# Optimization experiments

Hardware: AMD Instinct MI355X
Metric: run time of the kernel (lower is better)

The kernel has to match this reference:

```python
import jax, jax.numpy as jnp
import numpy as np

B, S, H = 2, 1024, 2048
E, I, K = 32, 768, 4


def setup_inputs() -> dict:
    key = jax.random.key(0)
    k1, k2, k3, k4, k5 = jax.random.split(key, 5)
    sH = 1.0 / np.sqrt(H)
    sI = 1.0 / np.sqrt(I)
    return {
        "hidden_states": jax.random.normal(k1, (B, S, H), dtype=jnp.float32),
        "gate_w": jax.random.normal(k2, (E, H), dtype=jnp.float32) * sH,
        "w_gate": jax.random.normal(k3, (E, H, I), dtype=jnp.float32) * sH,
        "w_up": jax.random.normal(k4, (E, H, I), dtype=jnp.float32) * sH,
        "w_down": jax.random.normal(k5, (E, I, H), dtype=jnp.float32) * sI,
        "top_k": K,
    }


def reference(hidden_states, gate_w, w_gate, w_up, w_down, top_k):
    b, s, h = hidden_states.shape
    x = hidden_states.reshape(-1, h)                      # [T, H]
    T = x.shape[0]

    # Router: logits -> softmax over experts -> top-k -> renormalize
    logits = x @ gate_w.T                                 # [T, E]
    probs = jax.nn.softmax(logits, axis=-1)
    topv, topi = jax.lax.top_k(probs, top_k)              # [T, K]
    topv = topv / jnp.sum(topv, axis=-1, keepdims=True)   # norm_topk_prob

    # Dense routing-weight matrix (zero except selected experts) [T, E]
    rw = jnp.zeros((T, probs.shape[-1]), dtype=x.dtype)
    rw = rw.at[jnp.arange(T)[:, None], topi].set(topv)

    # Expert SwiGLU MLPs, computed for all experts then masked-combined
    g = jnp.einsum('th,ehi->eti', x, w_gate)              # [E, T, I]
    u = jnp.einsum('th,ehi->eti', x, w_up)                # [E, T, I]
    act = jax.nn.silu(g) * u                              # [E, T, I]
    expert_out = jnp.einsum('eti,eih->eth', act, w_down)  # [E, T, H]

    out = jnp.einsum('te,eth->th', rw, expert_out)        # combine [T, H]
    return out.reshape(b, s, h).astype(hidden_states.dtype)
```

## Files before the change

### kernel.cpp

```cpp
#include <hip/hip_runtime.h>
#include <hip/hip_bf16.h>
#include <math.h>

typedef unsigned short u16;
typedef unsigned int u32;
typedef unsigned long long u64;
typedef short s16x8 __attribute__((ext_vector_type(8)));
typedef u32 u32x2 __attribute__((ext_vector_type(2)));
typedef u32 u32x4 __attribute__((ext_vector_type(4)));
typedef float f32x4 __attribute__((ext_vector_type(4)));

#define TTOK 2048
#define HDIM 2048
#define ENUM 32
#define IDIM 768
#define KTOP 4

#define WS_XB   0L
#define WS_ACT  8388608L
#define WS_TIDX 20971520L
#define WS_TW   (WS_TIDX + 32768L)
#define WS_CNT  (WS_TW + 32768L)
#define WS_OFFS (WS_CNT + 128L)
#define WS_CUR  (WS_OFFS + 256L)
#define WS_RTOK (WS_CUR + 128L)
#define WS_RW   (WS_RTOK + 32768L)

#define LDBW 20

__device__ __forceinline__ u16 f2bf(float f) {
  unsigned u = __builtin_bit_cast(unsigned, f);
  unsigned r = (u + 0x7fffu + ((u >> 16) & 1u)) >> 16;
  return (u16)r;
}

__device__ __forceinline__ u32 cvtpk(float lo, float hi) {
  u32 r;
  asm("v_cvt_pk_bf16_f32 %0, %1, %2" : "=v"(r) : "v"(lo), "v"(hi));
  return r;
}

__device__ __forceinline__ void gll16(const void* g, void* l) {
  u32 loff = __builtin_amdgcn_readfirstlane((u32)(u64)l);
  __builtin_amdgcn_global_load_lds(
      (const __attribute__((address_space(1))) u32*)(u64)g,
      (__attribute__((address_space(3))) u32*)loff, 16, 0, 0);
}

__device__ __forceinline__ s16x8 bfrag(const u32* B, int d0, int d1) {
  u32x2 lo = *(const u32x2*)(B + d0);
  u32x2 hi = *(const u32x2*)(B + d1);
  u32x4 v = {lo.x, lo.y, hi.x, hi.y};
  return __builtin_bit_cast(s16x8, v);
}

__global__ __launch_bounds__(256) void router_kernel(const float* __restrict__ x,
                                                     const float* __restrict__ gw,
                                                     u16* __restrict__ xb,
                                                     int* __restrict__ tidx,
                                                     float* __restrict__ tw,
                                                     int* __restrict__ counts) {
  __shared__ float xs[HDIM];
  __shared__ float part[256];
  __shared__ float lg[ENUM];
  int t = blockIdx.x;
  const float4* xr = (const float4*)(x + (long)t * HDIM);
  float4* xs4 = (float4*)xs;
  for (int i = threadIdx.x; i < HDIM / 4; i += 256) xs4[i] = xr[i];
  __syncthreads();
  {
    int i0 = threadIdx.x * 8;
    uint4 o;
    o.x = cvtpk(xs[i0], xs[i0 + 1]);
    o.y = cvtpk(xs[i0 + 2], xs[i0 + 3]);
    o.z = cvtpk(xs[i0 + 4], xs[i0 + 5]);
    o.w = cvtpk(xs[i0 + 6], xs[i0 + 7]);
    *(uint4*)(xb + (long)t * HDIM + i0) = o;
  }
  int e = threadIdx.x >> 3, ch = threadIdx.x & 7;
  const float4* gp = (const float4*)(gw + (long)e * HDIM + ch * 256);
  const float4* xp = (const float4*)(xs + ch * 256);
  float s = 0.f;
#pragma unroll 8
  for (int c = 0; c < 64; c++) {
    float4 gv = gp[c], xv = xp[c];
    s += gv.x * xv.x + gv.y * xv.y + gv.z * xv.z + gv.w * xv.w;
  }
  part[threadIdx.x] = s;
  __syncthreads();
  if (threadIdx.x < 32) {
    float v = 0.f;
#pragma unroll
    for (int j = 0; j < 8; j++) v += part[threadIdx.x * 8 + j];
    lg[threadIdx.x] = v;
  }
  __syncthreads();
  if (threadIdx.x == 0) {
    int sel[KTOP]; float sv[KTOP];
    unsigned mask = 0;
    for (int k = 0; k < KTOP; k++) {
      float best = -INFINITY; int bi = 0;
      for (int j = 0; j < ENUM; j++)
        if (!((mask >> j) & 1u) && lg[j] > best) { best = lg[j]; bi = j; }
      mask |= 1u << bi; sel[k] = bi; sv[k] = best;
    }
    float m = sv[0], den = 0.f, ex[KTOP];
    for (int k = 0; k < KTOP; k++) { ex[k] = expf(sv[k] - m); den += ex[k]; }
    for (int k = 0; k < KTOP; k++) {
      tidx[t * KTOP + k] = sel[k];
      tw[t * KTOP + k] = ex[k] / den;
      atomicAdd(&counts[sel[k]], 1);
    }
  }
}

__global__ void scan_kernel(const int* __restrict__ counts, int* __restrict__ offs,
                            int* __restrict__ cur) {
  if (threadIdx.x == 0) {
    int a = 0;
    for (int e = 0; e < ENUM; e++) { offs[e] = a; a += counts[e]; }
    offs[ENUM] = a;
  }
  if (threadIdx.x < ENUM) cur[threadIdx.x] = 0;
}

__global__ __launch_bounds__(256) void scatter_kernel(const int* __restrict__ tidx,
                                                      const float* __restrict__ tw,
                                                      const int* __restrict__ offs,
                                                      int* __restrict__ cur,
                                                      int* __restrict__ rtok,
                                                      float* __restrict__ rw) {
  int i = blockIdx.x * 256 + threadIdx.x;
  int e = tidx[i];
  int pos = atomicAdd(&cur[e], 1);
  int row = offs[e] + pos;
  rtok[row] = i >> 2;
  rw[row] = tw[i];
}

__global__ __launch_bounds__(512) void gemm1_kernel(const u16* __restrict__ xb,
                                                    const float* __restrict__ wgp,
                                                    const float* __restrict__ wup,
                                                    const int* __restrict__ offs,
                                                    const int* __restrict__ rtok,
                                                    u16* __restrict__ act) {
  int d = blockIdx.x;
  int e = d & 31;
  int nt = (d >> 5) % 12;
  int mt = d / 384;
  int off = offs[e], cnt = offs[e + 1] - off;
  int m0 = mt << 8;
  if (m0 >= cnt) return;
  int rows = cnt - m0; if (rows > 256) rows = 256;
  int baser = off + m0;
  int n0 = nt << 6;

  __shared__ __align__(16) u16 As[2][256 * 32];
  __shared__ __align__(16) u32 Bs[2][2][64 * LDBW];

  int tid = threadIdx.x;
  int ln = tid & 63, w = tid >> 6;
  int wm = w >> 1, wn = w & 1;
  int lhi = ln >> 4, llo = ln & 15;

  const u16* gA[2];
  int ldsA[2];
#pragma unroll
  for (int j = 0; j < 2; j++) {
    int idx = w * 2 + j;
    int r = idx * 16 + (ln >> 2);
    int c = ln & 3;
    int csrc = c ^ ((r >> 1) & 3);
    int rr = r < rows ? r : rows - 1;
    gA[j] = xb + (long)rtok[baser + rr] * HDIM + csrc * 8;
    ldsA[j] = idx * 1024;
  }

  int mat = tid >> 8;
  int t2 = tid & 255;
  int a = t2 & 15;
  int kk = t2 >> 4;
  const float* gB = (mat ? wup : wgp) + (long)e * ((long)HDIM * IDIM) +
                    (long)(2 * kk) * IDIM + n0 + 4 * a;
  int fB = 2 * (a & 7);
  int wOff[4];
#pragma unroll
  for (int j = 0; j < 4; j++) wOff[j] = (4 * a + j) * LDBW + (kk ^ fB);

  int offA[4];
#pragma unroll
  for (int mf = 0; mf < 4; mf++) {
    int r = wm * 64 + mf * 16 + llo;
    offA[mf] = r * 64 + ((lhi ^ ((r >> 1) & 3)) * 16);
  }
  int dB0[2], dB1[2];
#pragma unroll
  for (int nf = 0; nf < 2; nf++) {
    int n = wn * 32 + nf * 16 + llo;
    int f = 2 * ((n >> 2) & 7);
    dB0[nf] = n * LDBW + ((4 * lhi) ^ f);
    dB1[nf] = n * LDBW + (((4 * lhi) | 2) ^ f);
  }

  f32x4 accg[4][2], accu[4][2];
  f32x4 zz = {0.f, 0.f, 0.f, 0.f};
#pragma unroll
  for (int i = 0; i < 4; i++)
#pragma unroll
    for (int j = 0; j < 2; j++) { accg[i][j] = zz; accu[i][j] = zz; }

  float4 rB0, rB1;

  rB0 = *(const float4*)gB;
  rB1 = *(const float4*)(gB + IDIM);
  gll16(gA[0], (char*)As[0] + ldsA[0]);
  gll16(gA[1], (char*)As[0] + ldsA[1]);
  {
    u32* bb = &Bs[0][mat][0];
    bb[wOff[0]] = cvtpk(rB0.x, rB1.x);
    bb[wOff[1]] = cvtpk(rB0.y, rB1.y);
    bb[wOff[2]] = cvtpk(rB0.z, rB1.z);
    bb[wOff[3]] = cvtpk(rB0.w, rB1.w);
  }
  __syncthreads();

  const int NS = HDIM / 32;
  int buf = 0;
  for (int t = 0; t < NS; ++t) {
    if (t + 1 < NS) {
      const float* p = gB + (long)(t + 1) * 32 * IDIM;
      rB0 = *(const float4*)p;
      rB1 = *(const float4*)(p + IDIM);
      gll16(gA[0] + (t + 1) * 32, (char*)As[buf ^ 1] + ldsA[0]);
      gll16(gA[1] + (t + 1) * 32, (char*)As[buf ^ 1] + ldsA[1]);
    }
    __builtin_amdgcn_sched_barrier(0);
    {
      const char* Ab = (const char*)As[buf];
      const u32* Bg = &Bs[buf][0][0];
      const u32* Bu = &Bs[buf][1][0];
      s16x8 av[4];
#pragma unroll
      for (int mf = 0; mf < 4; mf++) av[mf] = *(const s16x8*)(Ab + offA[mf]);
#pragma unroll
      for (int nf = 0; nf < 2; nf++) {
        s16x8 bg = bfrag(Bg, dB0[nf], dB1[nf]);
        s16x8 bu = bfrag(Bu, dB0[nf], dB1[nf]);
#pragma unroll
        for (int mf = 0; mf < 4; mf++) {
          accg[mf][nf] = __builtin_amdgcn_mfma_f32_16x16x32_bf16(av[mf], bg, accg[mf][nf], 0, 0, 0);
          accu[mf][nf] = __builtin_amdgcn_mfma_f32_16x16x32_bf16(av[mf], bu, accu[mf][nf], 0, 0, 0);
        }
      }
    }
    if (t + 1 < NS) {
      u32* bb = &Bs[buf ^ 1][mat][0];
      bb[wOff[0]] = cvtpk(rB0.x, rB1.x);
      bb[wOff[1]] = cvtpk(rB0.y, rB1.y);
      bb[wOff[2]] = cvtpk(rB0.z, rB1.z);
      bb[wOff[3]] = cvtpk(rB0.w, rB1.w);
    }
    __syncthreads();
    buf ^= 1;
  }

  int rb = wm * 64 + lhi * 4;
  int cb = n0 + wn * 32 + llo;
#pragma unroll
  for (int mf = 0; mf < 4; mf++) {
#pragma unroll
    for (int r4 = 0; r4 < 4; r4++) {
      int rl = rb + mf * 16 + r4;
      if (rl < rows) {
        long rowb = (long)(baser + rl) * IDIM;
#pragma unroll
        for (int nf = 0; nf < 2; nf++) {
          float g = accg[mf][nf][r4], u = accu[mf][nf][r4];
          float av = g / (1.f + __expf(-g)) * u;
          act[rowb + cb + nf * 16] = f2bf(av);
        }
      }
    }
  }
}

__global__ __launch_bounds__(512) void gemm2_kernel(const u16* __restrict__ act,
                                                    const float* __restrict__ wdp,
                                                    const int* __restrict__ offs,
                                                    const int* __restrict__ rtok,
                                                    const float* __restrict__ rw,
                                                    float* __restrict__ out) {
  int d = blockIdx.x;
  int e = d & 31;
  int nt = (d >> 5) & 31;
  int mt = d >> 10;
  int off = offs[e], cnt = offs[e + 1] - off;
  int m0 = mt << 8;
  if (m0 >= cnt) return;
  int rows = cnt - m0; if (rows > 256) rows = 256;
  int baser = off + m0;
  int n0 = nt << 6;

  __shared__ __align__(16) u16 As[2][256 * 32];
  __shared__ __align__(16) u32 Bs[2][64 * LDBW];

  int tid = threadIdx.x;
  int ln = tid & 63, w = tid >> 6;
  int wm = w >> 1, wn = w & 1;
  int lhi = ln >> 4, llo = ln & 15;

  const u16* gA[2];
  int ldsA[2];
#pragma unroll
  for (int j = 0; j < 2; j++) {
    int idx = w * 2 + j;
    int r = idx * 16 + (ln >> 2);
    int c = ln & 3;
    int csrc = c ^ ((r >> 1) & 3);
    int rr = r < rows ? r : rows - 1;
    gA[j] = act + (long)(baser + rr) * IDIM + csrc * 8;
    ldsA[j] = idx * 1024;
  }

  int isB = (tid < 256);
  int a = tid & 15;
  int kk = (tid >> 4) & 15;
  const float* gB = wdp + (long)e * ((long)IDIM * HDIM) +
                    (long)(2 * kk) * HDIM + n0 + 4 * a;
  int fB = 2 * (a & 7);
  int wOff[4];
#pragma unroll
  for (int j = 0; j < 4; j++) wOff[j] = (4 * a + j) * LDBW + (kk ^ fB);

  int offA[4];
#pragma unroll
  for (int mf = 0; mf < 4; mf++) {
    int r = wm * 64 + mf * 16 + llo;
    offA[mf] = r * 64 + ((lhi ^ ((r >> 1) & 3)) * 16);
  }
  int dB0[2], dB1[2];
#pragma unroll
  for (int nf = 0; nf < 2; nf++) {
    int n = wn * 32 + nf * 16 + llo;
    int f = 2 * ((n >> 2) & 7);
    dB0[nf] = n * LDBW + ((4 * lhi) ^ f);
    dB1[nf] = n * LDBW + (((4 * lhi) | 2) ^ f);
  }

  f32x4 acc[4][2];
  f32x4 zz = {0.f, 0.f, 0.f, 0.f};
#pragma unroll
  for (int i = 0; i < 4; i++)
#pragma unroll
    for (int j = 0; j < 2; j++) acc[i][j] = zz;

  float4 rB0, rB1;

  if (isB) {
    rB0 = *(const float4*)gB;
    rB1 = *(const float4*)(gB + HDIM);
  }
  gll16(gA[0], (char*)As[0] + ldsA[0]);
  gll16(gA[1], (char*)As[0] + ldsA[1]);
  if (isB) {
    u32* bb = &Bs[0][0];
    bb[wOff[0]] = cvtpk(rB0.x, rB1.x);
    bb[wOff[1]] = cvtpk(rB0.y, rB1.y);
    bb[wOff[2]] = cvtpk(rB0.z, rB1.z);
    bb[wOff[3]] = cvtpk(rB0.w, rB1.w);
  }
  __syncthreads();

  const int NS = IDIM / 32;
  int buf = 0;
  for (int t = 0; t < NS; ++t) {
    if (t + 1 < NS) {
      if (isB) {
        const float* p = gB + (long)(t + 1) * 32 * HDIM;
        rB0 = *(const float4*)p;
        rB1 = *(const float4*)(p + HDIM);
      }
      gll16(gA[0] + (t + 1) * 32, (char*)As[buf ^ 1] + ldsA[0]);
      gll16(gA[1] + (t + 1) * 32, (char*)As[buf ^ 1] + ldsA[1]);
    }
    __builtin_amdgcn_sched_barrier(0);
    {
      const char* Ab = (const char*)As[buf];
      const u32* Bb = &Bs[buf][0];
      s16x8 av[4];
#pragma unroll
      for (int mf = 0; mf < 4; mf++) av[mf] = *(const s16x8*)(Ab + offA[mf]);
#pragma unroll
      for (int nf = 0; nf < 2; nf++) {
        s16x8 bv = bfrag(Bb, dB0[nf], dB1[nf]);
#pragma unroll
        for (int mf = 0; mf < 4; mf++)
          acc[mf][nf] = __builtin_amdgcn_mfma_f32_16x16x32_bf16(av[mf], bv, acc[mf][nf], 0, 0, 0);
      }
    }
    if (t + 1 < NS && isB) {
      u32* bb = &Bs[buf ^ 1][0];
      bb[wOff[0]] = cvtpk(rB0.x, rB1.x);
      bb[wOff[1]] = cvtpk(rB0.y, rB1.y);
      bb[wOff[2]] = cvtpk(rB0.z, rB1.z);
      bb[wOff[3]] = cvtpk(rB0.w, rB1.w);
    }
    __syncthreads();
    buf ^= 1;
  }

  int rb = wm * 64 + lhi * 4;
  int cb = n0 + wn * 32 + llo;
#pragma unroll
  for (int mf = 0; mf < 4; mf++) {
#pragma unroll
    for (int r4 = 0; r4 < 4; r4++) {
      int rl = rb + mf * 16 + r4;
      if (rl < rows) {
        int rr = baser + rl;
        float wt = rw[rr];
        long ob = (long)rtok[rr] * HDIM + cb;
        atomicAdd(&out[ob], acc[mf][0][r4] * wt);
        atomicAdd(&out[ob + 16], acc[mf][1][r4] * wt);
      }
    }
  }
}

extern "C" void kernel_launch(void* const* d_in, const int* in_sizes, int n_in,
                              void* d_out, int out_size, void* d_ws, size_t ws_size,
                              hipStream_t stream) {
  const float* x = (const float*)d_in[0];
  const float* gw = (const float*)d_in[1];
  const float* wgate = (const float*)d_in[2];
  const float* wup = (const float*)d_in[3];
  const float* wdown = (const float*)d_in[4];
  float* out = (float*)d_out;

  char* ws = (char*)d_ws;
  u16* xb = (u16*)(ws + WS_XB);
  u16* act = (u16*)(ws + WS_ACT);
  int* tidx = (int*)(ws + WS_TIDX);
  float* tw = (float*)(ws + WS_TW);
  int* cnt = (int*)(ws + WS_CNT);
  int* offs = (int*)(ws + WS_OFFS);
  int* cur = (int*)(ws + WS_CUR);
  int* rtok = (int*)(ws + WS_RTOK);
  float* rw = (float*)(ws + WS_RW);

  hipMemsetAsync(cnt, 0, 128, stream);
  hipMemsetAsync(d_out, 0, (size_t)out_size * sizeof(float), stream);

  hipLaunchKernelGGL(router_kernel, dim3(TTOK), dim3(256), 0, stream, x, gw, xb, tidx, tw, cnt);
  hipLaunchKernelGGL(scan_kernel, dim3(1), dim3(64), 0, stream, cnt, offs, cur);
  hipLaunchKernelGGL(scatter_kernel, dim3(TTOK * KTOP / 256), dim3(256), 0, stream, tidx, tw, offs, cur, rtok, rw);
  hipLaunchKernelGGL(gemm1_kernel, dim3(32 * 12 * 8), dim3(512), 0, stream, xb, wgate, wup, offs, rtok, act);
  hipLaunchKernelGGL(gemm2_kernel, dim3(32 * 32 * 8), dim3(512), 0, stream, act, wdown, offs, rtok, rw, out);
}
```

Baseline: 447.9 us.

## Triple-buffer A tiles with manual waitcnt and replace atomic combine with gather kernel

Both expert GEMMs now use a three-slot LDS ring for the A operand and an unrolled two-step loop with explicit vmcnt waits and raw barriers, so global loads run further ahead of the MFMA work. When the workspace is large enough, gemm2 writes per-row bf16 expert outputs instead of doing float atomics into the output. A new combine kernel then gathers each token's top-k rows via a row map and applies the routing weights, which also removes the output memset. The cost is extra LDS, an extra kernel launch, bf16 rounding of the expert outputs, and workspace-size-dependent control flow.

```diff
diff --git a/kernel.cpp b/kernel.cpp
--- a/kernel.cpp
+++ b/kernel.cpp
@@ -6,6 +6,7 @@
 typedef unsigned int u32;
 typedef unsigned long long u64;
 typedef short s16x8 __attribute__((ext_vector_type(8)));
+typedef u16 u16x8 __attribute__((ext_vector_type(8)));
 typedef u32 u32x2 __attribute__((ext_vector_type(2)));
 typedef u32 u32x4 __attribute__((ext_vector_type(4)));
 typedef float f32x4 __attribute__((ext_vector_type(4)));
@@ -25,6 +26,9 @@
 #define WS_CUR  (WS_OFFS + 256L)
 #define WS_RTOK (WS_CUR + 128L)
 #define WS_RW   (WS_RTOK + 32768L)
+#define WS_RMAP (WS_RW + 32768L)
+#define WS_EO   25165824L
+#define WS_NEED (WS_EO + 33554432L)
 
 #define LDBW 20
 
@@ -53,6 +57,19 @@
   u32x4 v = {lo.x, lo.y, hi.x, hi.y};
   return __builtin_bit_cast(s16x8, v);
 }
+
+#define WAIT_VM(N)                                            \
+  do {                                                        \
+    asm volatile("s_waitcnt vmcnt(" #N ")");                  \
+    __builtin_amdgcn_sched_barrier(0);                        \
+  } while (0)
+#define BARRIER()                                             \
+  do {                                                        \
+    asm volatile("s_waitcnt lgkmcnt(0)");                     \
+    __builtin_amdgcn_sched_barrier(0);                        \
+    __builtin_amdgcn_s_barrier();                             \
+    __builtin_amdgcn_sched_barrier(0);                        \
+  } while (0)
 
 __global__ __launch_bounds__(256) void router_kernel(const float* __restrict__ x,
                                                      const float* __restrict__ gw,
@@ -129,13 +146,15 @@
                                                       const int* __restrict__ offs,
                                                       int* __restrict__ cur,
                                                       int* __restrict__ rtok,
-                                                      float* __restrict__ rw) {
+                                                      float* __restrict__ rw,
+                                                      int* __restrict__ rowmap) {
   int i = blockIdx.x * 256 + threadIdx.x;
   int e = tidx[i];
   int pos = atomicAdd(&cur[e], 1);
   int row = offs[e] + pos;
   rtok[row] = i >> 2;
   rw[row] = tw[i];
+  rowmap[i] = row;
 }
 
 __global__ __launch_bounds__(512) void gemm1_kernel(const u16* __restrict__ xb,
@@ -155,7 +174,7 @@
   int baser = off + m0;
   int n0 = nt << 6;
 
-  __shared__ __align__(16) u16 As[2][256 * 32];
+  __shared__ __align__(16) u16 As[3][256 * 32];
   __shared__ __align__(16) u32 Bs[2][2][64 * LDBW];
 
   int tid = threadIdx.x;
@@ -209,59 +228,67 @@
 #pragma unroll
     for (int j = 0; j < 2; j++) { accg[i][j] = zz; accu[i][j] = zz; }
 
-  float4 rB0, rB1;
-
-  rB0 = *(const float4*)gB;
-  rB1 = *(const float4*)(gB + IDIM);
-  gll16(gA[0], (char*)As[0] + ldsA[0]);
-  gll16(gA[1], (char*)As[0] + ldsA[1]);
-  {
-    u32* bb = &Bs[0][mat][0];
-    bb[wOff[0]] = cvtpk(rB0.x, rB1.x);
-    bb[wOff[1]] = cvtpk(rB0.y, rB1.y);
-    bb[wOff[2]] = cvtpk(rB0.z, rB1.z);
-    bb[wOff[3]] = cvtpk(rB0.w, rB1.w);
-  }
-  __syncthreads();
+  float4 rbA0, rbA1, rbB0, rbB1;
+
+#define GLLA(pDst, tt)                                                \
+  { gll16(gA[0] + (tt) * 32, (char*)(pDst) + ldsA[0]);                \
+    gll16(gA[1] + (tt) * 32, (char*)(pDst) + ldsA[1]); }
+#define LDB1(r0, r1, tt)                                              \
+  { const float* p = gB + (long)(tt) * 32 * IDIM;                     \
+    r0 = *(const float4*)p; r1 = *(const float4*)(p + IDIM); }
+#define STB1(dstBs, r0, r1)                                           \
+  { u32* bb = &(dstBs)[mat][0];                                       \
+    bb[wOff[0]] = cvtpk(r0.x, r1.x);                                  \
+    bb[wOff[1]] = cvtpk(r0.y, r1.y);                                  \
+    bb[wOff[2]] = cvtpk(r0.z, r1.z);                                  \
+    bb[wOff[3]] = cvtpk(r0.w, r1.w); }
+#define COMP1(pA, bsel)                                               \
+  {                                                                   \
+    const char* Ab = (const char*)(pA);                               \
+    const u32* Bg = &Bs[bsel][0][0];                                  \
+    const u32* Bu = &Bs[bsel][1][0];                                  \
+    s16x8 av[4];                                                      \
+    _Pragma("unroll")                                                 \
+    for (int mf = 0; mf < 4; mf++) av[mf] = *(const s16x8*)(Ab + offA[mf]); \
+    _Pragma("unroll")                                                 \
+    for (int nf = 0; nf < 2; nf++) {                                  \
+      s16x8 bg = bfrag(Bg, dB0[nf], dB1[nf]);                         \
+      s16x8 bu = bfrag(Bu, dB0[nf], dB1[nf]);                         \
+      _Pragma("unroll")                                               \
+      for (int mf = 0; mf < 4; mf++) {                                \
+        accg[mf][nf] = __builtin_amdgcn_mfma_f32_16x16x32_bf16(av[mf], bg, accg[mf][nf], 0, 0, 0); \
+        accu[mf][nf] = __builtin_amdgcn_mfma_f32_16x16x32_bf16(av[mf], bu, accu[mf][nf], 0, 0, 0); \
+      }                                                               \
+    }                                                                 \
+  }
 
   const int NS = HDIM / 32;
-  int buf = 0;
-  for (int t = 0; t < NS; ++t) {
-    if (t + 1 < NS) {
-      const float* p = gB + (long)(t + 1) * 32 * IDIM;
-      rB0 = *(const float4*)p;
-      rB1 = *(const float4*)(p + IDIM);
-      gll16(gA[0] + (t + 1) * 32, (char*)As[buf ^ 1] + ldsA[0]);
-      gll16(gA[1] + (t + 1) * 32, (char*)As[buf ^ 1] + ldsA[1]);
-    }
-    __builtin_amdgcn_sched_barrier(0);
-    {
-      const char* Ab = (const char*)As[buf];
-      const u32* Bg = &Bs[buf][0][0];
-      const u32* Bu = &Bs[buf][1][0];
-      s16x8 av[4];
-#pragma unroll
-      for (int mf = 0; mf < 4; mf++) av[mf] = *(const s16x8*)(Ab + offA[mf]);
-#pragma unroll
-      for (int nf = 0; nf < 2; nf++) {
-        s16x8 bg = bfrag(Bg, dB0[nf], dB1[nf]);
-        s16x8 bu = bfrag(Bu, dB0[nf], dB1[nf]);
-#pragma unroll
-        for (int mf = 0; mf < 4; mf++) {
-          accg[mf][nf] = __builtin_amdgcn_mfma_f32_16x16x32_bf16(av[mf], bg, accg[mf][nf], 0, 0, 0);
-          accu[mf][nf] = __builtin_amdgcn_mfma_f32_16x16x32_bf16(av[mf], bu, accu[mf][nf], 0, 0, 0);
-        }
-      }
-    }
-    if (t + 1 < NS) {
-      u32* bb = &Bs[buf ^ 1][mat][0];
-      bb[wOff[0]] = cvtpk(rB0.x, rB1.x);
-      bb[wOff[1]] = cvtpk(rB0.y, rB1.y);
-      bb[wOff[2]] = cvtpk(rB0.z, rB1.z);
-      bb[wOff[3]] = cvtpk(rB0.w, rB1.w);
-    }
-    __syncthreads();
-    buf ^= 1;
+  u16 *pC = As[0], *pN = As[1], *pD = As[2];
+
+  GLLA(pC, 0); LDB1(rbA0, rbA1, 0);
+  GLLA(pN, 1); LDB1(rbB0, rbB1, 1);
+  __builtin_amdgcn_sched_barrier(0);
+  STB1(Bs[0], rbA0, rbA1);
+  WAIT_VM(4);
+  BARRIER();
+
+  for (int t = 0; t < NS; t += 2) {
+    if (t + 2 < NS) { GLLA(pD, t + 2); LDB1(rbA0, rbA1, t + 2); }
+    __builtin_amdgcn_sched_barrier(0);
+    COMP1(pC, 0);
+    __builtin_amdgcn_sched_barrier(0);
+    STB1(Bs[1], rbB0, rbB1);
+    if (t + 2 < NS) WAIT_VM(4); else WAIT_VM(0);
+    BARRIER();
+    { u16* tmp = pC; pC = pN; pN = pD; pD = tmp; }
+    if (t + 3 < NS) { GLLA(pD, t + 3); LDB1(rbB0, rbB1, t + 3); }
+    __builtin_amdgcn_sched_barrier(0);
+    COMP1(pC, 1);
+    __builtin_amdgcn_sched_barrier(0);
+    if (t + 2 < NS) STB1(Bs[0], rbA0, rbA1);
+    if (t + 3 < NS) WAIT_VM(4); else WAIT_VM(0);
+    if (t + 2 < NS) BARRIER();
+    { u16* tmp = pC; pC = pN; pN = pD; pD = tmp; }
   }
 
   int rb = wm * 64 + lhi * 4;
@@ -282,13 +309,19 @@
       }
     }
   }
-}
-
+#undef GLLA
+#undef LDB1
+#undef STB1
+#undef COMP1
+}
+
+template <int STORE>
 __global__ __launch_bounds__(512) void gemm2_kernel(const u16* __restrict__ act,
                                                     const float* __restrict__ wdp,
                                                     const int* __restrict__ offs,
                                                     const int* __restrict__ rtok,
                                                     const float* __restrict__ rw,
+                                                    u16* __restrict__ eo,
                                                     float* __restrict__ out) {
   int d = blockIdx.x;
   int e = d & 31;
@@ -301,7 +334,7 @@
   int baser = off + m0;
   int n0 = nt << 6;
 
-  __shared__ __align__(16) u16 As[2][256 * 32];
+  __shared__ __align__(16) u16 As[3][256 * 32];
   __shared__ __align__(16) u32 Bs[2][64 * LDBW];
 
   int tid = threadIdx.x;
@@ -354,59 +387,67 @@
 #pragma unroll
     for (int j = 0; j < 2; j++) acc[i][j] = zz;
 
-  float4 rB0, rB1;
-
-  if (isB) {
-    rB0 = *(const float4*)gB;
-    rB1 = *(const float4*)(gB + HDIM);
-  }
-  gll16(gA[0], (char*)As[0] + ldsA[0]);
-  gll16(gA[1], (char*)As[0] + ldsA[1]);
-  if (isB) {
-    u32* bb = &Bs[0][0];
-    bb[wOff[0]] = cvtpk(rB0.x, rB1.x);
-    bb[wOff[1]] = cvtpk(rB0.y, rB1.y);
-    bb[wOff[2]] = cvtpk(rB0.z, rB1.z);
-    bb[wOff[3]] = cvtpk(rB0.w, rB1.w);
-  }
-  __syncthreads();
+  float4 rbA0, rbA1, rbB0, rbB1;
+
+#define GLLA(pDst, tt)                                                \
+  { gll16(gA[0] + (tt) * 32, (char*)(pDst) + ldsA[0]);                \
+    gll16(gA[1] + (tt) * 32, (char*)(pDst) + ldsA[1]); }
+#define LDB2(r0, r1, tt)                                              \
+  { if (isB) {                                                        \
+      const float* p = gB + (long)(tt) * 32 * HDIM;                   \
+      r0 = *(const float4*)p; r1 = *(const float4*)(p + HDIM); } }
+#define STB2(dstBs, r0, r1)                                           \
+  { if (isB) {                                                        \
+      u32* bb = &(dstBs)[0];                                          \
+      bb[wOff[0]] = cvtpk(r0.x, r1.x);                                \
+      bb[wOff[1]] = cvtpk(r0.y, r1.y);                                \
+      bb[wOff[2]] = cvtpk(r0.z, r1.z);                                \
+      bb[wOff[3]] = cvtpk(r0.w, r1.w); } }
+#define WAITG2(nB, nNB)                                               \
+  { if (isB) WAIT_VM(nB); else WAIT_VM(nNB); }
+#define COMP2(pA, bsel)                                               \
+  {                                                                   \
+    const char* Ab = (const char*)(pA);                               \
+    const u32* Bb = &Bs[bsel][0];                                     \
+    s16x8 av[4];                                                      \
+    _Pragma("unroll")                                                 \
+    for (int mf = 0; mf < 4; mf++) av[mf] = *(const s16x8*)(Ab + offA[mf]); \
+    _Pragma("unroll")                                                 \
+    for (int nf = 0; nf < 2; nf++) {                                  \
+      s16x8 bv = bfrag(Bb, dB0[nf], dB1[nf]);                         \
+      _Pragma("unroll")                                               \
+      for (int mf = 0; mf < 4; mf++)                                  \
+        acc[mf][nf] = __builtin_amdgcn_mfma_f32_16x16x32_bf16(av[mf], bv, acc[mf][nf], 0, 0, 0); \
+    }                                                                 \
+  }
 
   const int NS = IDIM / 32;
-  int buf = 0;
-  for (int t = 0; t < NS; ++t) {
-    if (t + 1 < NS) {
-      if (isB) {
-        const float* p = gB + (long)(t + 1) * 32 * HDIM;
-        rB0 = *(const float4*)p;
-        rB1 = *(const float4*)(p + HDIM);
-      }
-      gll16(gA[0] + (t + 1) * 32, (char*)As[buf ^ 1] + ldsA[0]);
-      gll16(gA[1] + (t + 1) * 32, (char*)As[buf ^ 1] + ldsA[1]);
-    }
-    __builtin_amdgcn_sched_barrier(0);
-    {
-      const char* Ab = (const char*)As[buf];
-      const u32* Bb = &Bs[buf][0];
-      s16x8 av[4];
-#pragma unroll
-      for (int mf = 0; mf < 4; mf++) av[mf] = *(const s16x8*)(Ab + offA[mf]);
-#pragma unroll
-      for (int nf = 0; nf < 2; nf++) {
-        s16x8 bv = bfrag(Bb, dB0[nf], dB1[nf]);
-#pragma unroll
-        for (int mf = 0; mf < 4; mf++)
-          acc[mf][nf] = __builtin_amdgcn_mfma_f32_16x16x32_bf16(av[mf], bv, acc[mf][nf], 0, 0, 0);
-      }
-    }
-    if (t + 1 < NS && isB) {
-      u32* bb = &Bs[buf ^ 1][0];
-      bb[wOff[0]] = cvtpk(rB0.x, rB1.x);
-      bb[wOff[1]] = cvtpk(rB0.y, rB1.y);
-      bb[wOff[2]] = cvtpk(rB0.z, rB1.z);
-      bb[wOff[3]] = cvtpk(rB0.w, rB1.w);
-    }
-    __syncthreads();
-    buf ^= 1;
+  u16 *pC = As[0], *pN = As[1], *pD = As[2];
+
+  GLLA(pC, 0); LDB2(rbA0, rbA1, 0);
+  GLLA(pN, 1); LDB2(rbB0, rbB1, 1);
+  __builtin_amdgcn_sched_barrier(0);
+  STB2(Bs[0], rbA0, rbA1);
+  WAITG2(4, 2);
+  BARRIER();
+
+  for (int t = 0; t < NS; t += 2) {
+    if (t + 2 < NS) { GLLA(pD, t + 2); LDB2(rbA0, rbA1, t + 2); }
+    __builtin_amdgcn_sched_barrier(0);
+    COMP2(pC, 0);
+    __builtin_amdgcn_sched_barrier(0);
+    STB2(Bs[1], rbB0, rbB1);
+    if (t + 2 < NS) { WAITG2(4, 2); } else { WAIT_VM(0); }
+    BARRIER();
+    { u16* tmp = pC; pC = pN; pN = pD; pD = tmp; }
+    if (t + 3 < NS) { GLLA(pD, t + 3); LDB2(rbB0, rbB1, t + 3); }
+    __builtin_amdgcn_sched_barrier(0);
+    COMP2(pC, 1);
+    __builtin_amdgcn_sched_barrier(0);
+    if (t + 2 < NS) STB2(Bs[0], rbA0, rbA1);
+    if (t + 3 < NS) { WAITG2(4, 2); } else { WAIT_VM(0); }
+    if (t + 2 < NS) BARRIER();
+    { u16* tmp = pC; pC = pN; pN = pD; pD = tmp; }
   }
 
   int rb = wm * 64 + lhi * 4;
@@ -418,13 +459,46 @@
       int rl = rb + mf * 16 + r4;
       if (rl < rows) {
         int rr = baser + rl;
-        float wt = rw[rr];
-        long ob = (long)rtok[rr] * HDIM + cb;
-        atomicAdd(&out[ob], acc[mf][0][r4] * wt);
-        atomicAdd(&out[ob + 16], acc[mf][1][r4] * wt);
+        if (STORE) {
+          long ob = (long)rr * HDIM + cb;
+          eo[ob] = f2bf(acc[mf][0][r4]);
+          eo[ob + 16] = f2bf(acc[mf][1][r4]);
+        } else {
+          float wt = rw[rr];
+          long ob = (long)rtok[rr] * HDIM + cb;
+          atomicAdd(&out[ob], acc[mf][0][r4] * wt);
+          atomicAdd(&out[ob + 16], acc[mf][1][r4] * wt);
+        }
       }
     }
   }
+#undef GLLA
+#undef LDB2
+#undef STB2
+#undef WAITG2
+#undef COMP2
+}
+
+__global__ __launch_bounds__(256) void combine_kernel(const u16* __restrict__ eo,
+                                                      const int* __restrict__ rowmap,
+                                                      const float* __restrict__ tw,
+                                                      float* __restrict__ out) {
+  int t = blockIdx.x;
+  int h0 = threadIdx.x * 8;
+  float acc[8] = {0.f, 0.f, 0.f, 0.f, 0.f, 0.f, 0.f, 0.f};
+#pragma unroll
+  for (int k = 0; k < KTOP; k++) {
+    int r = rowmap[t * KTOP + k];
+    float wt = tw[t * KTOP + k];
+    u16x8 v = *(const u16x8*)(eo + (long)r * HDIM + h0);
+#pragma unroll
+    for (int j = 0; j < 8; j++)
+      acc[j] += wt * __builtin_bit_cast(float, ((u32)v[j]) << 16);
+  }
+  float4 o0 = {acc[0], acc[1], acc[2], acc[3]};
+  float4 o1 = {acc[4], acc[5], acc[6], acc[7]};
+  *(float4*)(out + (long)t * HDIM + h0) = o0;
+  *(float4*)(out + (long)t * HDIM + h0 + 4) = o1;
 }
 
 extern "C" void kernel_launch(void* const* d_in, const int* in_sizes, int n_in,
@@ -447,13 +521,22 @@
   int* cur = (int*)(ws + WS_CUR);
   int* rtok = (int*)(ws + WS_RTOK);
   float* rw = (float*)(ws + WS_RW);
+  int* rowmap = (int*)(ws + WS_RMAP);
+  u16* eo = (u16*)(ws + WS_EO);
+  bool storeMode = (ws_size >= (size_t)WS_NEED);
 
   hipMemsetAsync(cnt, 0, 128, stream);
-  hipMemsetAsync(d_out, 0, (size_t)out_size * sizeof(float), stream);
+  if (!storeMode)
+    hipMemsetAsync(d_out, 0, (size_t)out_size * sizeof(float), stream);
 
   hipLaunchKernelGGL(router_kernel, dim3(TTOK), dim3(256), 0, stream, x, gw, xb, tidx, tw, cnt);
   hipLaunchKernelGGL(scan_kernel, dim3(1), dim3(64), 0, stream, cnt, offs, cur);
-  hipLaunchKernelGGL(scatter_kernel, dim3(TTOK * KTOP / 256), dim3(256), 0, stream, tidx, tw, offs, cur, rtok, rw);
+  hipLaunchKernelGGL(scatter_kernel, dim3(TTOK * KTOP / 256), dim3(256), 0, stream, tidx, tw, offs, cur, rtok, rw, rowmap);
   hipLaunchKernelGGL(gemm1_kernel, dim3(32 * 12 * 8), dim3(512), 0, stream, xb, wgate, wup, offs, rtok, act);
-  hipLaunchKernelGGL(gemm2_kernel, dim3(32 * 32 * 8), dim3(512), 0, stream, act, wdown, offs, rtok, rw, out);
-}
+  if (storeMode) {
+    hipLaunchKernelGGL(gemm2_kernel<1>, dim3(32 * 32 * 8), dim3(512), 0, stream, act, wdown, offs, rtok, rw, eo, out);
+    hipLaunchKernelGGL(combine_kernel, dim3(TTOK), dim3(256), 0, stream, eo, rowmap, tw, out);
+  } else {
+    hipLaunchKernelGGL(gemm2_kernel<0>, dim3(32 * 32 * 8), dim3(512), 0, stream, act, wdown, offs, rtok, rw, eo, out);
+  }
+}
```

After: 444.2 us. No clear change (-0.8%).

## Retile expert GEMMs to 256x32 tiles, cap M tiles at two, add store+combine path

Applied to the files above, without the earlier changes.

Both expert GEMMs move from 512-thread 256x64 tiles to 256-thread 256x32 tiles. The grid now covers only two M tiles per expert, where it previously launched eight mostly empty ones, and block order is remapped so experts spread across XCD groups. The B LDS swizzle is dropped in favour of plain 16-byte fragment loads. When workspace allows, gemm2 writes bf16 per-row outputs and a combine kernel sums the top-k rows per token, replacing float atomics and the output memset. The cost is an extra bf16 rounding of expert outputs, possible LDS bank conflicts on B, and an implicit assumption that no expert gets more than 512 rows.

```diff
diff --git a/kernel.cpp b/kernel.cpp
--- a/kernel.cpp
+++ b/kernel.cpp
@@ -6,8 +6,7 @@
 typedef unsigned int u32;
 typedef unsigned long long u64;
 typedef short s16x8 __attribute__((ext_vector_type(8)));
-typedef u32 u32x2 __attribute__((ext_vector_type(2)));
-typedef u32 u32x4 __attribute__((ext_vector_type(4)));
+typedef u16 u16x8 __attribute__((ext_vector_type(8)));
 typedef float f32x4 __attribute__((ext_vector_type(4)));
 
 #define TTOK 2048
@@ -25,6 +24,9 @@
 #define WS_CUR  (WS_OFFS + 256L)
 #define WS_RTOK (WS_CUR + 128L)
 #define WS_RW   (WS_RTOK + 32768L)
+#define WS_RMAP (WS_RW + 32768L)
+#define WS_EO   25165824L
+#define WS_NEED (WS_EO + 33554432L)
 
 #define LDBW 20
 
@@ -45,13 +47,6 @@
   __builtin_amdgcn_global_load_lds(
       (const __attribute__((address_space(1))) u32*)(u64)g,
       (__attribute__((address_space(3))) u32*)loff, 16, 0, 0);
-}
-
-__device__ __forceinline__ s16x8 bfrag(const u32* B, int d0, int d1) {
-  u32x2 lo = *(const u32x2*)(B + d0);
-  u32x2 hi = *(const u32x2*)(B + d1);
-  u32x4 v = {lo.x, lo.y, hi.x, hi.y};
-  return __builtin_bit_cast(s16x8, v);
 }
 
 __global__ __launch_bounds__(256) void router_kernel(const float* __restrict__ x,
@@ -129,45 +124,48 @@
                                                       const int* __restrict__ offs,
                                                       int* __restrict__ cur,
                                                       int* __restrict__ rtok,
-                                                      float* __restrict__ rw) {
+                                                      float* __restrict__ rw,
+                                                      int* __restrict__ rowmap) {
   int i = blockIdx.x * 256 + threadIdx.x;
   int e = tidx[i];
   int pos = atomicAdd(&cur[e], 1);
   int row = offs[e] + pos;
   rtok[row] = i >> 2;
   rw[row] = tw[i];
-}
-
-__global__ __launch_bounds__(512) void gemm1_kernel(const u16* __restrict__ xb,
+  rowmap[i] = row;
+}
+
+__global__ __launch_bounds__(256) void gemm1_kernel(const u16* __restrict__ xb,
                                                     const float* __restrict__ wgp,
                                                     const float* __restrict__ wup,
                                                     const int* __restrict__ offs,
                                                     const int* __restrict__ rtok,
                                                     u16* __restrict__ act) {
   int d = blockIdx.x;
-  int e = d & 31;
-  int nt = (d >> 5) % 12;
-  int mt = d / 384;
+  int w = (d & 7) * 192 + (d >> 3);
+  int e = w / 48;
+  int rem = w % 48;
+  int nt = rem >> 1;
+  int mt = rem & 1;
   int off = offs[e], cnt = offs[e + 1] - off;
   int m0 = mt << 8;
   if (m0 >= cnt) return;
   int rows = cnt - m0; if (rows > 256) rows = 256;
   int baser = off + m0;
-  int n0 = nt << 6;
+  int n0 = nt << 5;
 
   __shared__ __align__(16) u16 As[2][256 * 32];
-  __shared__ __align__(16) u32 Bs[2][2][64 * LDBW];
+  __shared__ __align__(16) u32 Bs[2][2][32 * LDBW];
 
   int tid = threadIdx.x;
-  int ln = tid & 63, w = tid >> 6;
-  int wm = w >> 1, wn = w & 1;
+  int ln = tid & 63, wv = tid >> 6;
   int lhi = ln >> 4, llo = ln & 15;
 
-  const u16* gA[2];
-  int ldsA[2];
-#pragma unroll
-  for (int j = 0; j < 2; j++) {
-    int idx = w * 2 + j;
+  const u16* gA[4];
+  int ldsA[4];
+#pragma unroll
+  for (int j = 0; j < 4; j++) {
+    int idx = wv * 4 + j;
     int r = idx * 16 + (ln >> 2);
     int c = ln & 3;
     int csrc = c ^ ((r >> 1) & 3);
@@ -176,30 +174,27 @@
     ldsA[j] = idx * 1024;
   }
 
-  int mat = tid >> 8;
-  int t2 = tid & 255;
-  int a = t2 & 15;
-  int kk = t2 >> 4;
+  int mat = tid >> 7;
+  int t2 = tid & 127;
+  int qk = t2 & 15;
+  int g4 = t2 >> 4;
   const float* gB = (mat ? wup : wgp) + (long)e * ((long)HDIM * IDIM) +
-                    (long)(2 * kk) * IDIM + n0 + 4 * a;
-  int fB = 2 * (a & 7);
+                    (long)(2 * qk) * IDIM + n0 + 4 * g4;
   int wOff[4];
 #pragma unroll
-  for (int j = 0; j < 4; j++) wOff[j] = (4 * a + j) * LDBW + (kk ^ fB);
+  for (int j = 0; j < 4; j++) wOff[j] = (4 * g4 + j) * LDBW + qk;
 
   int offA[4];
 #pragma unroll
   for (int mf = 0; mf < 4; mf++) {
-    int r = wm * 64 + mf * 16 + llo;
-    offA[mf] = r * 64 + ((lhi ^ ((r >> 1) & 3)) * 16);
-  }
-  int dB0[2], dB1[2];
+    int r = wv * 64 + mf * 16 + llo;
+    offA[mf] = r * 64 + ((lhi ^ ((r >> 1) & 3)) << 4);
+  }
+  int offB[2];
 #pragma unroll
   for (int nf = 0; nf < 2; nf++) {
-    int n = wn * 32 + nf * 16 + llo;
-    int f = 2 * ((n >> 2) & 7);
-    dB0[nf] = n * LDBW + ((4 * lhi) ^ f);
-    dB1[nf] = n * LDBW + (((4 * lhi) | 2) ^ f);
+    int n = nf * 16 + llo;
+    offB[nf] = n * LDBW + lhi * 4;
   }
 
   f32x4 accg[4][2], accu[4][2];
@@ -211,41 +206,41 @@
 
   float4 rB0, rB1;
 
-  rB0 = *(const float4*)gB;
-  rB1 = *(const float4*)(gB + IDIM);
-  gll16(gA[0], (char*)As[0] + ldsA[0]);
-  gll16(gA[1], (char*)As[0] + ldsA[1]);
-  {
-    u32* bb = &Bs[0][mat][0];
-    bb[wOff[0]] = cvtpk(rB0.x, rB1.x);
-    bb[wOff[1]] = cvtpk(rB0.y, rB1.y);
-    bb[wOff[2]] = cvtpk(rB0.z, rB1.z);
-    bb[wOff[3]] = cvtpk(rB0.w, rB1.w);
-  }
+#define GLLA(buf, tt)                                                 \
+  { _Pragma("unroll")                                                 \
+    for (int j = 0; j < 4; j++)                                       \
+      gll16(gA[j] + (tt) * 32, (char*)As[buf] + ldsA[j]); }
+#define LDB(tt)                                                       \
+  { const float* p = gB + (long)(tt) * 32 * IDIM;                     \
+    rB0 = *(const float4*)p; rB1 = *(const float4*)(p + IDIM); }
+#define STB(buf)                                                      \
+  { u32* bb = &Bs[buf][mat][0];                                       \
+    bb[wOff[0]] = cvtpk(rB0.x, rB1.x);                                \
+    bb[wOff[1]] = cvtpk(rB0.y, rB1.y);                                \
+    bb[wOff[2]] = cvtpk(rB0.z, rB1.z);                                \
+    bb[wOff[3]] = cvtpk(rB0.w, rB1.w); }
+
+  const int NS = HDIM / 32;
+  LDB(0);
+  GLLA(0, 0);
+  STB(0);
   __syncthreads();
 
-  const int NS = HDIM / 32;
-  int buf = 0;
   for (int t = 0; t < NS; ++t) {
-    if (t + 1 < NS) {
-      const float* p = gB + (long)(t + 1) * 32 * IDIM;
-      rB0 = *(const float4*)p;
-      rB1 = *(const float4*)(p + IDIM);
-      gll16(gA[0] + (t + 1) * 32, (char*)As[buf ^ 1] + ldsA[0]);
-      gll16(gA[1] + (t + 1) * 32, (char*)As[buf ^ 1] + ldsA[1]);
-    }
+    int cur = t & 1;
+    if (t + 1 < NS) { LDB(t + 1); GLLA(cur ^ 1, t + 1); }
     __builtin_amdgcn_sched_barrier(0);
     {
-      const char* Ab = (const char*)As[buf];
-      const u32* Bg = &Bs[buf][0][0];
-      const u32* Bu = &Bs[buf][1][0];
+      const char* Ab = (const char*)As[cur];
+      const u32* Bg = &Bs[cur][0][0];
+      const u32* Bu = &Bs[cur][1][0];
       s16x8 av[4];
 #pragma unroll
       for (int mf = 0; mf < 4; mf++) av[mf] = *(const s16x8*)(Ab + offA[mf]);
 #pragma unroll
       for (int nf = 0; nf < 2; nf++) {
-        s16x8 bg = bfrag(Bg, dB0[nf], dB1[nf]);
-        s16x8 bu = bfrag(Bu, dB0[nf], dB1[nf]);
+        s16x8 bg = *(const s16x8*)(Bg + offB[nf]);
+        s16x8 bu = *(const s16x8*)(Bu + offB[nf]);
 #pragma unroll
         for (int mf = 0; mf < 4; mf++) {
           accg[mf][nf] = __builtin_amdgcn_mfma_f32_16x16x32_bf16(av[mf], bg, accg[mf][nf], 0, 0, 0);
@@ -253,19 +248,12 @@
         }
       }
     }
-    if (t + 1 < NS) {
-      u32* bb = &Bs[buf ^ 1][mat][0];
-      bb[wOff[0]] = cvtpk(rB0.x, rB1.x);
-      bb[wOff[1]] = cvtpk(rB0.y, rB1.y);
-      bb[wOff[2]] = cvtpk(rB0.z, rB1.z);
-      bb[wOff[3]] = cvtpk(rB0.w, rB1.w);
-    }
+    if (t + 1 < NS) STB(cur ^ 1);
     __syncthreads();
-    buf ^= 1;
-  }
-
-  int rb = wm * 64 + lhi * 4;
-  int cb = n0 + wn * 32 + llo;
+  }
+
+  int rb = wv * 64 + lhi * 4;
+  int cb = n0 + llo;
 #pragma unroll
   for (int mf = 0; mf < 4; mf++) {
 #pragma unroll
@@ -282,38 +270,44 @@
       }
     }
   }
-}
-
-__global__ __launch_bounds__(512) void gemm2_kernel(const u16* __restrict__ act,
+#undef GLLA
+#undef LDB
+#undef STB
+}
+
+template <int STORE>
+__global__ __launch_bounds__(256) void gemm2_kernel(const u16* __restrict__ act,
                                                     const float* __restrict__ wdp,
                                                     const int* __restrict__ offs,
                                                     const int* __restrict__ rtok,
                                                     const float* __restrict__ rw,
+                                                    u16* __restrict__ eo,
                                                     float* __restrict__ out) {
   int d = blockIdx.x;
-  int e = d & 31;
-  int nt = (d >> 5) & 31;
-  int mt = d >> 10;
+  int w = (d & 7) * 512 + (d >> 3);
+  int e = w / 128;
+  int rem = w % 128;
+  int nt = rem >> 1;
+  int mt = rem & 1;
   int off = offs[e], cnt = offs[e + 1] - off;
   int m0 = mt << 8;
   if (m0 >= cnt) return;
   int rows = cnt - m0; if (rows > 256) rows = 256;
   int baser = off + m0;
-  int n0 = nt << 6;
+  int n0 = nt << 5;
 
   __shared__ __align__(16) u16 As[2][256 * 32];
-  __shared__ __align__(16) u32 Bs[2][64 * LDBW];
+  __shared__ __align__(16) u32 Bs[2][32 * LDBW];
 
   int tid = threadIdx.x;
-  int ln = tid & 63, w = tid >> 6;
-  int wm = w >> 1, wn = w & 1;
+  int ln = tid & 63, wv = tid >> 6;
   int lhi = ln >> 4, llo = ln & 15;
 
-  const u16* gA[2];
-  int ldsA[2];
-#pragma unroll
-  for (int j = 0; j < 2; j++) {
-    int idx = w * 2 + j;
+  const u16* gA[4];
+  int ldsA[4];
+#pragma unroll
+  for (int j = 0; j < 4; j++) {
+    int idx = wv * 4 + j;
     int r = idx * 16 + (ln >> 2);
     int c = ln & 3;
     int csrc = c ^ ((r >> 1) & 3);
@@ -322,29 +316,26 @@
     ldsA[j] = idx * 1024;
   }
 
-  int isB = (tid < 256);
-  int a = tid & 15;
-  int kk = (tid >> 4) & 15;
+  int isB = (tid < 128);
+  int qk = tid & 15;
+  int g4 = (tid >> 4) & 7;
   const float* gB = wdp + (long)e * ((long)IDIM * HDIM) +
-                    (long)(2 * kk) * HDIM + n0 + 4 * a;
-  int fB = 2 * (a & 7);
+                    (long)(2 * qk) * HDIM + n0 + 4 * g4;
   int wOff[4];
 #pragma unroll
-  for (int j = 0; j < 4; j++) wOff[j] = (4 * a + j) * LDBW + (kk ^ fB);
+  for (int j = 0; j < 4; j++) wOff[j] = (4 * g4 + j) * LDBW + qk;
 
   int offA[4];
 #pragma unroll
   for (int mf = 0; mf < 4; mf++) {
-    int r = wm * 64 + mf * 16 + llo;
-    offA[mf] = r * 64 + ((lhi ^ ((r >> 1) & 3)) * 16);
-  }
-  int dB0[2], dB1[2];
+    int r = wv * 64 + mf * 16 + llo;
+    offA[mf] = r * 64 + ((lhi ^ ((r >> 1) & 3)) << 4);
+  }
+  int offB[2];
 #pragma unroll
   for (int nf = 0; nf < 2; nf++) {
-    int n = wn * 32 + nf * 16 + llo;
-    int f = 2 * ((n >> 2) & 7);
-    dB0[nf] = n * LDBW + ((4 * lhi) ^ f);
-    dB1[nf] = n * LDBW + (((4 * lhi) | 2) ^ f);
+    int n = nf * 16 + llo;
+    offB[nf] = n * LDBW + lhi * 4;
   }
 
   f32x4 acc[4][2];
@@ -356,61 +347,52 @@
 
   float4 rB0, rB1;
 
-  if (isB) {
-    rB0 = *(const float4*)gB;
-    rB1 = *(const float4*)(gB + HDIM);
-  }
-  gll16(gA[0], (char*)As[0] + ldsA[0]);
-  gll16(gA[1], (char*)As[0] + ldsA[1]);
-  if (isB) {
-    u32* bb = &Bs[0][0];
-    bb[wOff[0]] = cvtpk(rB0.x, rB1.x);
-    bb[wOff[1]] = cvtpk(rB0.y, rB1.y);
-    bb[wOff[2]] = cvtpk(rB0.z, rB1.z);
-    bb[wOff[3]] = cvtpk(rB0.w, rB1.w);
-  }
+#define GLLA(buf, tt)                                                 \
+  { _Pragma("unroll")                                                 \
+    for (int j = 0; j < 4; j++)                                       \
+      gll16(gA[j] + (tt) * 32, (char*)As[buf] + ldsA[j]); }
+#define LDB(tt)                                                       \
+  { if (isB) {                                                        \
+      const float* p = gB + (long)(tt) * 32 * HDIM;                   \
+      rB0 = *(const float4*)p; rB1 = *(const float4*)(p + HDIM); } }
+#define STB(buf)                                                      \
+  { if (isB) {                                                        \
+      u32* bb = &Bs[buf][0];                                          \
+      bb[wOff[0]] = cvtpk(rB0.x, rB1.x);                              \
+      bb[wOff[1]] = cvtpk(rB0.y, rB1.y);                              \
+      bb[wOff[2]] = cvtpk(rB0.z, rB1.z);                              \
+      bb[wOff[3]] = cvtpk(rB0.w, rB1.w); } }
+
+  const int NS = IDIM / 32;
+  LDB(0);
+  GLLA(0, 0);
+  STB(0);
   __syncthreads();
 
-  const int NS = IDIM / 32;
-  int buf = 0;
   for (int t = 0; t < NS; ++t) {
-    if (t + 1 < NS) {
-      if (isB) {
-        const float* p = gB + (long)(t + 1) * 32 * HDIM;
-        rB0 = *(const float4*)p;
-        rB1 = *(const float4*)(p + HDIM);
-      }
-      gll16(gA[0] + (t + 1) * 32, (char*)As[buf ^ 1] + ldsA[0]);
-      gll16(gA[1] + (t + 1) * 32, (char*)As[buf ^ 1] + ldsA[1]);
-    }
+    int cur = t & 1;
+    if (t + 1 < NS) { LDB(t + 1); GLLA(cur ^ 1, t + 1); }
     __builtin_amdgcn_sched_barrier(0);
     {
-      const char* Ab = (const char*)As[buf];
-      const u32* Bb = &Bs[buf][0];
+      const char* Ab = (const char*)As[cur];
+      const u32* Bb = &Bs[cur][0];
       s16x8 av[4];
 #pragma unroll
       for (int mf = 0; mf < 4; mf++) av[mf] = *(const s16x8*)(Ab + offA[mf]);
 #pragma unroll
       for (int nf = 0; nf < 2; nf++) {
-        s16x8 bv = bfrag(Bb, dB0[nf], dB1[nf]);
+        s16x8 bv = *(const s16x8*)(Bb + offB[nf]);
 #pragma unroll
         for (int mf = 0; mf < 4; mf++)
           acc[mf][nf] = __builtin_amdgcn_mfma_f32_16x16x32_bf16(av[mf], bv, acc[mf][nf], 0, 0, 0);
       }
     }
-    if (t + 1 < NS && isB) {
-      u32* bb = &Bs[buf ^ 1][0];
-      bb[wOff[0]] = cvtpk(rB0.x, rB1.x);
-      bb[wOff[1]] = cvtpk(rB0.y, rB1.y);
-      bb[wOff[2]] = cvtpk(rB0.z, rB1.z);
-      bb[wOff[3]] = cvtpk(rB0.w, rB1.w);
-    }
+    if (t + 1 < NS) STB(cur ^ 1);
     __syncthreads();
-    buf ^= 1;
-  }
-
-  int rb = wm * 64 + lhi * 4;
-  int cb = n0 + wn * 32 + llo;
+  }
+
+  int rb = wv * 64 + lhi * 4;
+  int cb = n0 + llo;
 #pragma unroll
   for (int mf = 0; mf < 4; mf++) {
 #pragma unroll
@@ -418,13 +400,44 @@
       int rl = rb + mf * 16 + r4;
       if (rl < rows) {
         int rr = baser + rl;
-        float wt = rw[rr];
-        long ob = (long)rtok[rr] * HDIM + cb;
-        atomicAdd(&out[ob], acc[mf][0][r4] * wt);
-        atomicAdd(&out[ob + 16], acc[mf][1][r4] * wt);
+        if (STORE) {
+          long ob = (long)rr * HDIM + cb;
+          eo[ob] = f2bf(acc[mf][0][r4]);
+          eo[ob + 16] = f2bf(acc[mf][1][r4]);
+        } else {
+          float wt = rw[rr];
+          long ob = (long)rtok[rr] * HDIM + cb;
+          atomicAdd(&out[ob], acc[mf][0][r4] * wt);
+          atomicAdd(&out[ob + 16], acc[mf][1][r4] * wt);
+        }
       }
     }
   }
+#undef GLLA
+#undef LDB
+#undef STB
+}
+
+__global__ __launch_bounds__(256) void combine_kernel(const u16* __restrict__ eo,
+                                                      const int* __restrict__ rowmap,
+                                                      const float* __restrict__ tw,
+                                                      float* __restrict__ out) {
+  int t = blockIdx.x;
+  int h0 = threadIdx.x * 8;
+  float acc[8] = {0.f, 0.f, 0.f, 0.f, 0.f, 0.f, 0.f, 0.f};
+#pragma unroll
+  for (int k = 0; k < KTOP; k++) {
+    int r = rowmap[t * KTOP + k];
+    float wt = tw[t * KTOP + k];
+    u16x8 v = *(const u16x8*)(eo + (long)r * HDIM + h0);
+#pragma unroll
+    for (int j = 0; j < 8; j++)
+      acc[j] += wt * __builtin_bit_cast(float, ((u32)v[j]) << 16);
+  }
+  float4 o0 = {acc[0], acc[1], acc[2], acc[3]};
+  float4 o1 = {acc[4], acc[5], acc[6], acc[7]};
+  *(float4*)(out + (long)t * HDIM + h0) = o0;
+  *(float4*)(out + (long)t * HDIM + h0 + 4) = o1;
 }
 
 extern "C" void kernel_launch(void* const* d_in, const int* in_sizes, int n_in,
@@ -447,13 +460,22 @@
   int* cur = (int*)(ws + WS_CUR);
   int* rtok = (int*)(ws + WS_RTOK);
   float* rw = (float*)(ws + WS_RW);
+  int* rowmap = (int*)(ws + WS_RMAP);
+  u16* eo = (u16*)(ws + WS_EO);
+  bool storeMode = (ws_size >= (size_t)WS_NEED);
 
   hipMemsetAsync(cnt, 0, 128, stream);
-  hipMemsetAsync(d_out, 0, (size_t)out_size * sizeof(float), stream);
+  if (!storeMode)
+    hipMemsetAsync(d_out, 0, (size_t)out_size * sizeof(float), stream);
 
   hipLaunchKernelGGL(router_kernel, dim3(TTOK), dim3(256), 0, stream, x, gw, xb, tidx, tw, cnt);
   hipLaunchKernelGGL(scan_kernel, dim3(1), dim3(64), 0, stream, cnt, offs, cur);
-  hipLaunchKernelGGL(scatter_kernel, dim3(TTOK * KTOP / 256), dim3(256), 0, stream, tidx, tw, offs, cur, rtok, rw);
-  hipLaunchKernelGGL(gemm1_kernel, dim3(32 * 12 * 8), dim3(512), 0, stream, xb, wgate, wup, offs, rtok, act);
-  hipLaunchKernelGGL(gemm2_kernel, dim3(32 * 32 * 8), dim3(512), 0, stream, act, wdown, offs, rtok, rw, out);
-}
+  hipLaunchKernelGGL(scatter_kernel, dim3(TTOK * KTOP / 256), dim3(256), 0, stream, tidx, tw, offs, cur, rtok, rw, rowmap);
+  hipLaunchKernelGGL(gemm1_kernel, dim3(32 * 24 * 2), dim3(256), 0, stream, xb, wgate, wup, offs, rtok, act);
+  if (storeMode) {
+    hipLaunchKernelGGL(gemm2_kernel<1>, dim3(32 * 64 * 2), dim3(256), 0, stream, act, wdown, offs, rtok, rw, eo, out);
+    hipLaunchKernelGGL(combine_kernel, dim3(TTOK), dim3(256), 0, stream, eo, rowmap, tw, out);
+  } else {
+    hipLaunchKernelGGL(gemm2_kernel<0>, dim3(32 * 64 * 2), dim3(256), 0, stream, act, wdown, offs, rtok, rw, eo, out);
+  }
+}
```

Measured after the change: 611.6 us. +36.5%, slower.

## Replace atomic scatter-add in down-projection with bf16 store plus gather combine

Applied to the files above, without the earlier changes.

The down-projection GEMM now writes per-row expert outputs as bf16 into a workspace buffer instead of doing weighted fp32 atomicAdds into the output. A new combine kernel gathers the top-k rows for each token through a row map and writes the weighted sum directly, which removes the output memset and the atomic contention. This adds an extra 16 MB write and read plus an additional bf16 rounding of the expert outputs. The new path runs only when the workspace is large enough; otherwise the atomic path is kept.

```diff
diff --git a/kernel.cpp b/kernel.cpp
--- a/kernel.cpp
+++ b/kernel.cpp
@@ -6,6 +6,7 @@
 typedef unsigned int u32;
 typedef unsigned long long u64;
 typedef short s16x8 __attribute__((ext_vector_type(8)));
+typedef u16 u16x8 __attribute__((ext_vector_type(8)));
 typedef u32 u32x2 __attribute__((ext_vector_type(2)));
 typedef u32 u32x4 __attribute__((ext_vector_type(4)));
 typedef float f32x4 __attribute__((ext_vector_type(4)));
@@ -25,6 +26,9 @@
 #define WS_CUR  (WS_OFFS + 256L)
 #define WS_RTOK (WS_CUR + 128L)
 #define WS_RW   (WS_RTOK + 32768L)
+#define WS_RMAP (WS_RW + 32768L)
+#define WS_EO   25165824L
+#define WS_NEED (WS_EO + 33554432L)
 
 #define LDBW 20
 
@@ -129,13 +133,15 @@
                                                       const int* __restrict__ offs,
                                                       int* __restrict__ cur,
                                                       int* __restrict__ rtok,
-                                                      float* __restrict__ rw) {
+                                                      float* __restrict__ rw,
+                                                      int* __restrict__ rowmap) {
   int i = blockIdx.x * 256 + threadIdx.x;
   int e = tidx[i];
   int pos = atomicAdd(&cur[e], 1);
   int row = offs[e] + pos;
   rtok[row] = i >> 2;
   rw[row] = tw[i];
+  rowmap[i] = row;
 }
 
 __global__ __launch_bounds__(512) void gemm1_kernel(const u16* __restrict__ xb,
@@ -284,11 +290,13 @@
   }
 }
 
+template <int STORE>
 __global__ __launch_bounds__(512) void gemm2_kernel(const u16* __restrict__ act,
                                                     const float* __restrict__ wdp,
                                                     const int* __restrict__ offs,
                                                     const int* __restrict__ rtok,
                                                     const float* __restrict__ rw,
+                                                    u16* __restrict__ eo,
                                                     float* __restrict__ out) {
   int d = blockIdx.x;
   int e = d & 31;
@@ -418,13 +426,41 @@
       int rl = rb + mf * 16 + r4;
       if (rl < rows) {
         int rr = baser + rl;
-        float wt = rw[rr];
-        long ob = (long)rtok[rr] * HDIM + cb;
-        atomicAdd(&out[ob], acc[mf][0][r4] * wt);
-        atomicAdd(&out[ob + 16], acc[mf][1][r4] * wt);
+        if (STORE) {
+          long ob = (long)rr * HDIM + cb;
+          eo[ob] = f2bf(acc[mf][0][r4]);
+          eo[ob + 16] = f2bf(acc[mf][1][r4]);
+        } else {
+          float wt = rw[rr];
+          long ob = (long)rtok[rr] * HDIM + cb;
+          atomicAdd(&out[ob], acc[mf][0][r4] * wt);
+          atomicAdd(&out[ob + 16], acc[mf][1][r4] * wt);
+        }
       }
     }
   }
+}
+
+__global__ __launch_bounds__(256) void combine_kernel(const u16* __restrict__ eo,
+                                                      const int* __restrict__ rowmap,
+                                                      const float* __restrict__ tw,
+                                                      float* __restrict__ out) {
+  int t = blockIdx.x;
+  int h0 = threadIdx.x * 8;
+  float acc[8] = {0.f, 0.f, 0.f, 0.f, 0.f, 0.f, 0.f, 0.f};
+#pragma unroll
+  for (int k = 0; k < KTOP; k++) {
+    int r = rowmap[t * KTOP + k];
+    float wt = tw[t * KTOP + k];
+    u16x8 v = *(const u16x8*)(eo + (long)r * HDIM + h0);
+#pragma unroll
+    for (int j = 0; j < 8; j++)
+      acc[j] += wt * __builtin_bit_cast(float, ((u32)v[j]) << 16);
+  }
+  float4 o0 = {acc[0], acc[1], acc[2], acc[3]};
+  float4 o1 = {acc[4], acc[5], acc[6], acc[7]};
+  *(float4*)(out + (long)t * HDIM + h0) = o0;
+  *(float4*)(out + (long)t * HDIM + h0 + 4) = o1;
 }
 
 extern "C" void kernel_launch(void* const* d_in, const int* in_sizes, int n_in,
@@ -447,13 +483,22 @@
   int* cur = (int*)(ws + WS_CUR);
   int* rtok = (int*)(ws + WS_RTOK);
   float* rw = (float*)(ws + WS_RW);
+  int* rowmap = (int*)(ws + WS_RMAP);
+  u16* eo = (u16*)(ws + WS_EO);
+  bool storeMode = (ws_size >= (size_t)WS_NEED);
 
   hipMemsetAsync(cnt, 0, 128, stream);
-  hipMemsetAsync(d_out, 0, (size_t)out_size * sizeof(float), stream);
+  if (!storeMode)
+    hipMemsetAsync(d_out, 0, (size_t)out_size * sizeof(float), stream);
 
   hipLaunchKernelGGL(router_kernel, dim3(TTOK), dim3(256), 0, stream, x, gw, xb, tidx, tw, cnt);
   hipLaunchKernelGGL(scan_kernel, dim3(1), dim3(64), 0, stream, cnt, offs, cur);
-  hipLaunchKernelGGL(scatter_kernel, dim3(TTOK * KTOP / 256), dim3(256), 0, stream, tidx, tw, offs, cur, rtok, rw);
+  hipLaunchKernelGGL(scatter_kernel, dim3(TTOK * KTOP / 256), dim3(256), 0, stream, tidx, tw, offs, cur, rtok, rw, rowmap);
   hipLaunchKernelGGL(gemm1_kernel, dim3(32 * 12 * 8), dim3(512), 0, stream, xb, wgate, wup, offs, rtok, act);
-  hipLaunchKernelGGL(gemm2_kernel, dim3(32 * 32 * 8), dim3(512), 0, stream, act, wdown, offs, rtok, rw, out);
-}
+  if (storeMode) {
+    hipLaunchKernelGGL(gemm2_kernel<1>, dim3(32 * 32 * 8), dim3(512), 0, stream, act, wdown, offs, rtok, rw, eo, out);
+    hipLaunchKernelGGL(combine_kernel, dim3(TTOK), dim3(256), 0, stream, eo, rowmap, tw, out);
+  } else {
+    hipLaunchKernelGGL(gemm2_kernel<0>, dim3(32 * 32 * 8), dim3(512), 0, stream, act, wdown, offs, rtok, rw, eo, out);
+  }
+}
```

Result: faster. 396.6 us (-11.4%).
